# Kernel optimization log

Hardware: AMD Instinct MI355X
Metric: run time of the kernel (lower is better)

Reference implementation:

```python
import jax, jax.numpy as jnp
import numpy as np

CPV = 64  # cpv_size; output_size = CPV*(CPV+1)//2 = 2080

def _tri_indices(cpv):
    # Reproduce the torch nested-loop scatter order:
    # for idx_x in range(cpv): for idx_y in range(cpv-idx_x): col = cpv-1-idx_y
    rows = np.repeat(np.arange(cpv), cpv - np.arange(cpv))
    cols = np.concatenate([np.arange(cpv - 1, i - 1, -1) for i in range(cpv)])
    return jnp.asarray(rows), jnp.asarray(cols)


def setup_inputs() -> dict:
    key = jax.random.key(0)
    ks = jax.random.split(key, 12)
    B, D_in, H, L = 8192, 1024, 2048, CPV * (CPV + 1) // 2
    s = lambda fan_in: 1.0 / np.sqrt(fan_in)
    return {
        "x":   jax.random.normal(ks[0], (B, D_in), jnp.float32),
        "W1":  jax.random.uniform(ks[1], (D_in, H), jnp.float32, -s(D_in), s(D_in)),
        "b1":  jnp.zeros((H,), jnp.float32),
        "W2":  jax.random.uniform(ks[2], (H, H), jnp.float32, -s(H), s(H)),
        "b2":  jnp.zeros((H,), jnp.float32),
        "W21": jax.random.uniform(ks[3], (H, H), jnp.float32, -s(H), s(H)),
        "b21": jnp.zeros((H,), jnp.float32),
        "W22": jax.random.uniform(ks[4], (H, H), jnp.float32, -s(H), s(H)),
        "b22": jnp.zeros((H,), jnp.float32),
        "W3":  jax.random.uniform(ks[5], (H, L), jnp.float32, -s(H), s(H)),
        "b3":  jnp.zeros((L,), jnp.float32),
    }


def reference(x, W1, b1, W2, b2, W21, b21, W22, b22, W3, b3):
    lrelu = lambda t: jax.nn.leaky_relu(t, 0.01)
    h = lrelu(x @ W1 + b1)
    h = lrelu(h @ W2 + b2)
    h = lrelu(h @ W21 + b21)
    h = lrelu(h @ W22 + b22)
    y = h @ W3 + b3  # [B, L] with L = CPV*(CPV+1)//2
    rows, cols = _tri_indices(CPV)
    is_diag = rows == cols  # diagonal entries are abs'ed (negated when <= 0)
    vals = jnp.where(is_diag[None, :] & (y <= 0), -y, y)
    B = y.shape[0]
    M = jnp.zeros((B, CPV, CPV), y.dtype).at[:, rows, cols].set(vals)
    return jnp.transpose(M, (1, 2, 0))  # torch stacks per-example matrices on dim=2
```

## Files before the change

### kernel.cpp

```cpp
#include <hip/hip_runtime.h>
#include <hip/hip_bf16.h>
#include <stdint.h>

typedef short short8 __attribute__((ext_vector_type(8)));
typedef float f32x4  __attribute__((ext_vector_type(4)));

typedef __attribute__((address_space(1))) uint32_t u32_g;
typedef __attribute__((address_space(3))) uint32_t u32_l;

#define BM 128
#define BN 128
#define BK 64

__device__ __forceinline__ void gld_lds16(const void* g, const void* l) {
  __builtin_amdgcn_global_load_lds((u32_g*)(uintptr_t)g, (u32_l*)(uintptr_t)l, 16, 0, 0);
}

template <int FINAL>
__global__ __launch_bounds__(256) void gemm_k(
    const __hip_bfloat16* __restrict__ A,
    const __hip_bfloat16* __restrict__ BT,
    const float* __restrict__ bias,
    __hip_bfloat16* __restrict__ Cb,
    float* __restrict__ Cf,
    const int* __restrict__ tbl,
    int K, int Nreal)
{
  __shared__ __attribute__((aligned(16))) __hip_bfloat16 As[BM * BK];
  __shared__ __attribute__((aligned(16))) __hip_bfloat16 Bs[BN * BK];

  const int tid  = threadIdx.x;
  const int lane = tid & 63;
  const int l15  = lane & 15;
  const int quad = lane >> 4;
  const int wave = tid >> 6;
  const int wm   = (wave >> 1) << 6;
  const int wn   = (wave & 1) << 6;

  const int bm = blockIdx.x * BM;
  const int bn = blockIdx.y * BN;

  const __hip_bfloat16* ag[4];
  const __hip_bfloat16* bg[4];
  uint32_t lofs[4];
#pragma unroll
  for (int c = 0; c < 4; ++c) {
    int ci   = tid + 256 * c;
    int row  = ci >> 3;
    int chk  = ci & 7;
    int gchk = chk ^ (row & 7);
    ag[c]   = A  + (size_t)(bm + row) * K + gchk * 8;
    bg[c]   = BT + (size_t)(bn + row) * K + gchk * 8;
    lofs[c] = (uint32_t)ci * 16u;
  }

  f32x4 acc[4][4];
#pragma unroll
  for (int i = 0; i < 4; ++i)
#pragma unroll
    for (int j = 0; j < 4; ++j)
      acc[i][j] = (f32x4){0.f, 0.f, 0.f, 0.f};

  const int nk = K >> 6;
  for (int kt = 0; kt < nk; ++kt) {
#pragma unroll
    for (int c = 0; c < 4; ++c) {
      gld_lds16(ag[c], (const char*)As + lofs[c]);
      gld_lds16(bg[c], (const char*)Bs + lofs[c]);
      ag[c] += BK;
      bg[c] += BK;
    }
    __syncthreads();
#pragma unroll
    for (int ks = 0; ks < 2; ++ks) {
      short8 af[4], bf[4];
      const int cf = ks * 4 + quad;
#pragma unroll
      for (int i = 0; i < 4; ++i) {
        int m  = wm + i * 16 + l15;
        int sc = cf ^ (m & 7);
        af[i]  = *(const short8*)(As + m * BK + sc * 8);
      }
#pragma unroll
      for (int j = 0; j < 4; ++j) {
        int n  = wn + j * 16 + l15;
        int sc = cf ^ (n & 7);
        bf[j]  = *(const short8*)(Bs + n * BK + sc * 8);
      }
#pragma unroll
      for (int i = 0; i < 4; ++i)
#pragma unroll
        for (int j = 0; j < 4; ++j)
          acc[i][j] = __builtin_amdgcn_mfma_f32_16x16x32_bf16(af[i], bf[j], acc[i][j], 0, 0, 0);
    }
    __syncthreads();
  }

  if (FINAL == 0) {
#pragma unroll
    for (int j = 0; j < 4; ++j) {
      int   n  = bn + wn + j * 16 + l15;
      float bv = bias[n];
#pragma unroll
      for (int i = 0; i < 4; ++i) {
        int m0 = bm + wm + i * 16 + quad * 4;
#pragma unroll
        for (int r = 0; r < 4; ++r) {
          float v = acc[i][j][r] + bv;
          v = (v > 0.f) ? v : 0.01f * v;
          Cb[(size_t)(m0 + r) * 2048 + n] = __float2bfloat16(v);
        }
      }
    }
  } else {
#pragma unroll
    for (int j = 0; j < 4; ++j) {
      int n = bn + wn + j * 16 + l15;
      if (n < Nreal) {
        float bv   = bias[n];
        int  code  = tbl[n];
        int  dst   = code & 4095;
        bool diag  = (code & 4096) != 0;
#pragma unroll
        for (int i = 0; i < 4; ++i) {
          int m0 = bm + wm + i * 16 + quad * 4;
          f32x4 pk;
#pragma unroll
          for (int r = 0; r < 4; ++r) {
            float v = acc[i][j][r] + bv;
            if (diag) v = fabsf(v);
            pk[r] = v;
          }
          *reinterpret_cast<f32x4*>(Cf + (size_t)dst * 8192 + m0) = pk;
        }
      }
    }
  }
}

__global__ void transpose_k(const float* __restrict__ in,
                            __hip_bfloat16* __restrict__ out,
                            int K, int N)
{
  __shared__ __hip_bfloat16 t[32][33];
  const int n0 = blockIdx.x * 32;
  const int k0 = blockIdx.y * 32;
  const int tx = threadIdx.x, ty = threadIdx.y;
  const __hip_bfloat16 zero = __float2bfloat16(0.f);
#pragma unroll
  for (int r = 0; r < 32; r += 8) {
    int k = k0 + ty + r, n = n0 + tx;
    t[ty + r][tx] = (n < N) ? __float2bfloat16(in[(size_t)k * N + n]) : zero;
  }
  __syncthreads();
#pragma unroll
  for (int r = 0; r < 32; r += 8) {
    int n = n0 + ty + r;
    out[(size_t)n * K + k0 + tx] = t[tx][ty + r];
  }
}

__global__ void cvt_k(const float* __restrict__ in,
                      __hip_bfloat16* __restrict__ out, int n)
{
  int i = (blockIdx.x * 256 + threadIdx.x) * 4;
  if (i >= n) return;
  float4 v = *reinterpret_cast<const float4*>(in + i);
  union { unsigned short us[4]; uint2 v2; } pk;
  __hip_bfloat16 h;
  h = __float2bfloat16(v.x); pk.us[0] = *reinterpret_cast<unsigned short*>(&h);
  h = __float2bfloat16(v.y); pk.us[1] = *reinterpret_cast<unsigned short*>(&h);
  h = __float2bfloat16(v.z); pk.us[2] = *reinterpret_cast<unsigned short*>(&h);
  h = __float2bfloat16(v.w); pk.us[3] = *reinterpret_cast<unsigned short*>(&h);
  *reinterpret_cast<uint2*>(out + i) = pk.v2;
}

__global__ void table_k(int* __restrict__ tbl)
{
  int l = blockIdx.x * 64 + threadIdx.x;
  if (l >= 2080) return;
  int r = 0, s = 0;
  while (s + (64 - r) <= l) { s += 64 - r; ++r; }
  int c = 63 - (l - s);
  tbl[l] = (r * 64 + c) | ((r == c) ? 4096 : 0);
}

extern "C" void kernel_launch(void* const* d_in, const int* in_sizes, int n_in,
                              void* d_out, int out_size, void* d_ws, size_t ws_size,
                              hipStream_t stream)
{
  const float* x   = (const float*)d_in[0];
  const float* W1  = (const float*)d_in[1];
  const float* b1  = (const float*)d_in[2];
  const float* W2  = (const float*)d_in[3];
  const float* b2  = (const float*)d_in[4];
  const float* W21 = (const float*)d_in[5];
  const float* b21 = (const float*)d_in[6];
  const float* W22 = (const float*)d_in[7];
  const float* b22 = (const float*)d_in[8];
  const float* W3  = (const float*)d_in[9];
  const float* b3  = (const float*)d_in[10];
  float* out = (float*)d_out;

  char* ws = (char*)d_ws;
  __hip_bfloat16* act0 = (__hip_bfloat16*)(ws);
  __hip_bfloat16* act1 = (__hip_bfloat16*)(ws + ((size_t)32 << 20));
  __hip_bfloat16* xb   = act1;
  __hip_bfloat16* W1T  = (__hip_bfloat16*)(ws + ((size_t)64 << 20));
  __hip_bfloat16* W2T  = (__hip_bfloat16*)(ws + ((size_t)68 << 20));
  __hip_bfloat16* W21T = (__hip_bfloat16*)(ws + ((size_t)76 << 20));
  __hip_bfloat16* W22T = (__hip_bfloat16*)(ws + ((size_t)84 << 20));
  __hip_bfloat16* W3T  = (__hip_bfloat16*)(ws + ((size_t)92 << 20));
  int*            tbl  = (int*)(ws + ((size_t)101 << 20));

  hipMemsetAsync(d_out, 0, (size_t)out_size * sizeof(float), stream);
  table_k<<<33, 64, 0, stream>>>(tbl);

  cvt_k<<<8192, 256, 0, stream>>>(x, xb, 8192 * 1024);

  dim3 tb(32, 8);
  transpose_k<<<dim3(64, 32), tb, 0, stream>>>(W1,  W1T,  1024, 2048);
  transpose_k<<<dim3(64, 64), tb, 0, stream>>>(W2,  W2T,  2048, 2048);
  transpose_k<<<dim3(64, 64), tb, 0, stream>>>(W21, W21T, 2048, 2048);
  transpose_k<<<dim3(64, 64), tb, 0, stream>>>(W22, W22T, 2048, 2048);
  transpose_k<<<dim3(68, 64), tb, 0, stream>>>(W3,  W3T,  2048, 2080);

  gemm_k<0><<<dim3(64, 16), 256, 0, stream>>>(xb,   W1T,  b1,  act0, nullptr, nullptr, 1024, 2048);
  gemm_k<0><<<dim3(64, 16), 256, 0, stream>>>(act0, W2T,  b2,  act1, nullptr, nullptr, 2048, 2048);
  gemm_k<0><<<dim3(64, 16), 256, 0, stream>>>(act1, W21T, b21, act0, nullptr, nullptr, 2048, 2048);
  gemm_k<0><<<dim3(64, 16), 256, 0, stream>>>(act0, W22T, b22, act1, nullptr, nullptr, 2048, 2048);
  gemm_k<1><<<dim3(64, 17), 256, 0, stream>>>(act1, W3T,  b3,  nullptr, out,  tbl,     2048, 2080);
}
```

Baseline: 615.8 us.

## Use 32x32x16 MFMA for hidden GEMMs and zero only the lower triangle

The four hidden-layer GEMMs move from 16x16x32 bf16 MFMA tiles to 32x32x16 MFMA tiles with a 2x2 per-wave accumulator layout. This halves the instruction count and cuts LDS fragment reads per FLOP. The full-output memset is replaced by a kernel that zeroes only the 2016 strictly-lower-triangular positions that the final GEMM never writes. The risk is that the 32x32 epilogue scatters 2-byte bf16 stores across rows with poorer coalescing.

```diff
diff --git a/kernel.cpp b/kernel.cpp
--- a/kernel.cpp
+++ b/kernel.cpp
@@ -2,8 +2,9 @@
 #include <hip/hip_bf16.h>
 #include <stdint.h>
 
-typedef short short8 __attribute__((ext_vector_type(8)));
-typedef float f32x4  __attribute__((ext_vector_type(4)));
+typedef short short8  __attribute__((ext_vector_type(8)));
+typedef float f32x4   __attribute__((ext_vector_type(4)));
+typedef float f32x16  __attribute__((ext_vector_type(16)));
 
 typedef __attribute__((address_space(1))) uint32_t u32_g;
 typedef __attribute__((address_space(3))) uint32_t u32_l;
@@ -16,23 +17,20 @@
   __builtin_amdgcn_global_load_lds((u32_g*)(uintptr_t)g, (u32_l*)(uintptr_t)l, 16, 0, 0);
 }
 
-template <int FINAL>
-__global__ __launch_bounds__(256) void gemm_k(
+__global__ __launch_bounds__(256) void gemm32_k(
     const __hip_bfloat16* __restrict__ A,
     const __hip_bfloat16* __restrict__ BT,
     const float* __restrict__ bias,
-    __hip_bfloat16* __restrict__ Cb,
-    float* __restrict__ Cf,
-    const int* __restrict__ tbl,
-    int K, int Nreal)
+    __hip_bfloat16* __restrict__ C,
+    int K)
 {
   __shared__ __attribute__((aligned(16))) __hip_bfloat16 As[BM * BK];
   __shared__ __attribute__((aligned(16))) __hip_bfloat16 Bs[BN * BK];
 
   const int tid  = threadIdx.x;
   const int lane = tid & 63;
-  const int l15  = lane & 15;
-  const int quad = lane >> 4;
+  const int l31  = lane & 31;
+  const int half = lane >> 5;
   const int wave = tid >> 6;
   const int wm   = (wave >> 1) << 6;
   const int wn   = (wave & 1) << 6;
@@ -54,12 +52,12 @@
     lofs[c] = (uint32_t)ci * 16u;
   }
 
-  f32x4 acc[4][4];
-#pragma unroll
-  for (int i = 0; i < 4; ++i)
-#pragma unroll
-    for (int j = 0; j < 4; ++j)
-      acc[i][j] = (f32x4){0.f, 0.f, 0.f, 0.f};
+  f32x16 acc[2][2];
+#pragma unroll
+  for (int i = 0; i < 2; ++i)
+#pragma unroll
+    for (int j = 0; j < 2; ++j)
+      acc[i][j] = (f32x16)(0.f);
 
   const int nk = K >> 6;
   for (int kt = 0; kt < nk; ++kt) {
@@ -72,20 +70,109 @@
     }
     __syncthreads();
 #pragma unroll
+    for (int kk = 0; kk < 4; ++kk) {
+      short8 af[2], bf[2];
+      const int cf = kk * 2 + half;
+#pragma unroll
+      for (int t = 0; t < 2; ++t) {
+        int m  = wm + t * 32 + l31;
+        af[t]  = *(const short8*)(As + m * BK + (cf ^ (m & 7)) * 8);
+        int n  = wn + t * 32 + l31;
+        bf[t]  = *(const short8*)(Bs + n * BK + (cf ^ (n & 7)) * 8);
+      }
+#pragma unroll
+      for (int ti = 0; ti < 2; ++ti)
+#pragma unroll
+        for (int tj = 0; tj < 2; ++tj)
+          acc[ti][tj] = __builtin_amdgcn_mfma_f32_32x32x16_bf16(af[ti], bf[tj], acc[ti][tj], 0, 0, 0);
+    }
+    __syncthreads();
+  }
+
+#pragma unroll
+  for (int tj = 0; tj < 2; ++tj) {
+    int   n  = bn + wn + tj * 32 + l31;
+    float bv = bias[n];
+#pragma unroll
+    for (int ti = 0; ti < 2; ++ti) {
+      int base = bm + wm + ti * 32 + 4 * half;
+#pragma unroll
+      for (int reg = 0; reg < 16; ++reg) {
+        int m   = base + (reg & 3) + 8 * (reg >> 2);
+        float v = acc[ti][tj][reg] + bv;
+        v = (v > 0.f) ? v : 0.01f * v;
+        C[(size_t)m * 2048 + n] = __float2bfloat16(v);
+      }
+    }
+  }
+}
+
+__global__ __launch_bounds__(256) void gemm16f_k(
+    const __hip_bfloat16* __restrict__ A,
+    const __hip_bfloat16* __restrict__ BT,
+    const float* __restrict__ bias,
+    float* __restrict__ Cf,
+    const int* __restrict__ tbl,
+    int K, int Nreal)
+{
+  __shared__ __attribute__((aligned(16))) __hip_bfloat16 As[BM * BK];
+  __shared__ __attribute__((aligned(16))) __hip_bfloat16 Bs[BN * BK];
+
+  const int tid  = threadIdx.x;
+  const int lane = tid & 63;
+  const int l15  = lane & 15;
+  const int quad = lane >> 4;
+  const int wave = tid >> 6;
+  const int wm   = (wave >> 1) << 6;
+  const int wn   = (wave & 1) << 6;
+
+  const int bm = blockIdx.x * BM;
+  const int bn = blockIdx.y * BN;
+
+  const __hip_bfloat16* ag[4];
+  const __hip_bfloat16* bg[4];
+  uint32_t lofs[4];
+#pragma unroll
+  for (int c = 0; c < 4; ++c) {
+    int ci   = tid + 256 * c;
+    int row  = ci >> 3;
+    int chk  = ci & 7;
+    int gchk = chk ^ (row & 7);
+    ag[c]   = A  + (size_t)(bm + row) * K + gchk * 8;
+    bg[c]   = BT + (size_t)(bn + row) * K + gchk * 8;
+    lofs[c] = (uint32_t)ci * 16u;
+  }
+
+  f32x4 acc[4][4];
+#pragma unroll
+  for (int i = 0; i < 4; ++i)
+#pragma unroll
+    for (int j = 0; j < 4; ++j)
+      acc[i][j] = (f32x4){0.f, 0.f, 0.f, 0.f};
+
+  const int nk = K >> 6;
+  for (int kt = 0; kt < nk; ++kt) {
+#pragma unroll
+    for (int c = 0; c < 4; ++c) {
+      gld_lds16(ag[c], (const char*)As + lofs[c]);
+      gld_lds16(bg[c], (const char*)Bs + lofs[c]);
+      ag[c] += BK;
+      bg[c] += BK;
+    }
+    __syncthreads();
+#pragma unroll
     for (int ks = 0; ks < 2; ++ks) {
       short8 af[4], bf[4];
       const int cf = ks * 4 + quad;
 #pragma unroll
       for (int i = 0; i < 4; ++i) {
         int m  = wm + i * 16 + l15;
-        int sc = cf ^ (m & 7);
-        af[i]  = *(const short8*)(As + m * BK + sc * 8);
+        af[i]  = *(const short8*)(As + m * BK + ((cf ^ (m & 7)) * 8));
       }
 #pragma unroll
       for (int j = 0; j < 4; ++j) {
         int n  = wn + j * 16 + l15;
-        int sc = cf ^ (n & 7);
-        bf[j]  = *(const short8*)(Bs + n * BK + sc * 8);
+        bf[j]  = *(const short8*)(Bs + n * BK + ((cf ^ (n & 7)) * 8));
       }
 #pragma unroll
       for (int i = 0; i < 4; ++i)
@@ -96,43 +183,25 @@
     __syncthreads();
   }
 
-  if (FINAL == 0) {
-#pragma unroll
-    for (int j = 0; j < 4; ++j) {
-      int   n  = bn + wn + j * 16 + l15;
-      float bv = bias[n];
+#pragma unroll
+  for (int j = 0; j < 4; ++j) {
+    int n = bn + wn + j * 16 + l15;
+    if (n < Nreal) {
+      float bv   = bias[n];
+      int  code  = tbl[n];
+      int  dst   = code & 4095;
+      bool diag  = (code & 4096) != 0;
 #pragma unroll
       for (int i = 0; i < 4; ++i) {
         int m0 = bm + wm + i * 16 + quad * 4;
+        f32x4 pk;
 #pragma unroll
         for (int r = 0; r < 4; ++r) {
           float v = acc[i][j][r] + bv;
-          v = (v > 0.f) ? v : 0.01f * v;
-          Cb[(size_t)(m0 + r) * 2048 + n] = __float2bfloat16(v);
+          if (diag) v = fabsf(v);
+          pk[r] = v;
         }
-      }
-    }
-  } else {
-#pragma unroll
-    for (int j = 0; j < 4; ++j) {
-      int n = bn + wn + j * 16 + l15;
-      if (n < Nreal) {
-        float bv   = bias[n];
-        int  code  = tbl[n];
-        int  dst   = code & 4095;
-        bool diag  = (code & 4096) != 0;
-#pragma unroll
-        for (int i = 0; i < 4; ++i) {
-          int m0 = bm + wm + i * 16 + quad * 4;
-          f32x4 pk;
-#pragma unroll
-          for (int r = 0; r < 4; ++r) {
-            float v = acc[i][j][r] + bv;
-            if (diag) v = fabsf(v);
-            pk[r] = v;
-          }
-          *reinterpret_cast<f32x4*>(Cf + (size_t)dst * 8192 + m0) = pk;
-        }
+        *reinterpret_cast<f32x4*>(Cf + (size_t)dst * 8192 + m0) = pk;
       }
     }
   }
@@ -183,6 +252,20 @@
   while (s + (64 - r) <= l) { s += 64 - r; ++r; }
   int c = 63 - (l - s);
   tbl[l] = (r * 64 + c) | ((r == c) ? 4096 : 0);
+}
+
+__global__ void zlo_k(float* __restrict__ out)
+{
+  int p = blockIdx.x;
+  int r = (int)((1.0f + sqrtf(1.0f + 8.0f * (float)p)) * 0.5f);
+  while (r * (r - 1) / 2 > p) --r;
+  while ((r + 1) * r / 2 <= p) ++r;
+  int c = p - r * (r - 1) / 2;
+  float* dst = out + (size_t)(r * 64 + c) * 8192;
+  f32x4 z = (f32x4){0.f, 0.f, 0.f, 0.f};
+#pragma unroll
+  for (int i = 0; i < 8; ++i)
+    *reinterpret_cast<f32x4*>(dst + i * 1024 + threadIdx.x * 4) = z;
 }
 
 extern "C" void kernel_launch(void* const* d_in, const int* in_sizes, int n_in,
@@ -213,8 +296,8 @@
   __hip_bfloat16* W3T  = (__hip_bfloat16*)(ws + ((size_t)92 << 20));
   int*            tbl  = (int*)(ws + ((size_t)101 << 20));
 
-  hipMemsetAsync(d_out, 0, (size_t)out_size * sizeof(float), stream);
   table_k<<<33, 64, 0, stream>>>(tbl);
+  zlo_k<<<2016, 256, 0, stream>>>(out);
 
   cvt_k<<<8192, 256, 0, stream>>>(x, xb, 8192 * 1024);
 
@@ -225,9 +308,9 @@
   transpose_k<<<dim3(64, 64), tb, 0, stream>>>(W22, W22T, 2048, 2048);
   transpose_k<<<dim3(68, 64), tb, 0, stream>>>(W3,  W3T,  2048, 2080);
 
-  gemm_k<0><<<dim3(64, 16), 256, 0, stream>>>(xb,   W1T,  b1,  act0, nullptr, nullptr, 1024, 2048);
-  gemm_k<0><<<dim3(64, 16), 256, 0, stream>>>(act0, W2T,  b2,  act1, nullptr, nullptr, 2048, 2048);
-  gemm_k<0><<<dim3(64, 16), 256, 0, stream>>>(act1, W21T, b21, act0, nullptr, nullptr, 2048, 2048);
-  gemm_k<0><<<dim3(64, 16), 256, 0, stream>>>(act0, W22T, b22, act1, nullptr, nullptr, 2048, 2048);
-  gemm_k<1><<<dim3(64, 17), 256, 0, stream>>>(act1, W3T,  b3,  nullptr, out,  tbl,     2048, 2080);
-}
+  gemm32_k<<<dim3(64, 16), 256, 0, stream>>>(xb,   W1T,  b1,  act0, 1024);
+  gemm32_k<<<dim3(64, 16), 256, 0, stream>>>(act0, W2T,  b2,  act1, 2048);
+  gemm32_k<<<dim3(64, 16), 256, 0, stream>>>(act1, W21T, b21, act0, 2048);
+  gemm32_k<<<dim3(64, 16), 256, 0, stream>>>(act0, W22T, b22, act1, 2048);
+  gemm16f_k<<<dim3(64, 17), 256, 0, stream>>>(act1, W3T, b3, out, tbl, 2048, 2080);
+}
```

New measurement: 642.4 us. 4.3% more time.
